# Performance work log

Measured on AMD Instinct MI355X. Metric: run time of the kernel, lower is better.

The kernel has to match this reference:

```python
import jax, jax.numpy as jnp
import numpy as np

N = 100000   # nodes
E = 1600000  # edges (avg degree 16)
F = 64       # input feature dim
H = 64       # hidden dim
O = 64       # conv output dim
C = 2        # channels (x.shape[1])
S = 1000     # number of subgraphs
M = 64       # nodes per subgraph
MH = 128     # MLP hidden
OUT = 1      # MLP output


def setup_inputs() -> dict:
    key = jax.random.key(0)
    ks = jax.random.split(key, 16)
    x = jax.random.normal(ks[0], (N, C, F), jnp.float32)
    edge_index = jax.random.randint(ks[1], (2, E), 0, N, dtype=jnp.int32)
    edge_weight = jax.random.uniform(ks[2], (E,), jnp.float32)
    subG_node = jax.random.randint(ks[3], (S, M), 0, N, dtype=jnp.int32)
    s1 = 1.0 / np.sqrt(F)
    s2 = 1.0 / np.sqrt(H)
    sm1 = 1.0 / np.sqrt(O)
    sm2 = 1.0 / np.sqrt(MH)
    return {
        "x": x,
        "edge_index": edge_index,
        "edge_weight": edge_weight,
        "subG_node": subG_node,
        "W1": jax.random.normal(ks[4], (F, H), jnp.float32) * s1,
        "b1": jnp.zeros((H,), jnp.float32),
        "gn_w": jnp.ones((H,), jnp.float32),
        "gn_b": jnp.zeros((H,), jnp.float32),
        "gn_ms": jnp.ones((H,), jnp.float32),
        "W2": jax.random.normal(ks[5], (H, O), jnp.float32) * s2,
        "b2": jnp.zeros((O,), jnp.float32),
        "mW1": jax.random.normal(ks[6], (O, MH), jnp.float32) * sm1,
        "mb1": jnp.zeros((MH,), jnp.float32),
        "mW2": jax.random.normal(ks[7], (MH, OUT), jnp.float32) * sm2,
        "mb2": jnp.zeros((OUT,), jnp.float32),
    }


def _graph_norm(h, w, b, ms, eps=1e-5):
    # PyG GraphNorm over all nodes (single graph): per-feature stats
    mean = jnp.mean(h, axis=0, keepdims=True)
    out = h - ms * mean
    var = jnp.mean(out * out, axis=0, keepdims=True)
    return w * out * jax.lax.rsqrt(var + eps) + b


def _gcn_layer(h, src, dst, norm, self_norm, W, b, n):
    # GCNConv: h' = D^-1/2 (A + I) D^-1/2 (h @ W) + b
    hw = h @ W                                   # [N, out]
    msg = norm[:, None] * hw[src]                # [E, out] gather
    agg = jax.ops.segment_sum(msg, dst, num_segments=n)  # scatter-add
    agg = agg + self_norm[:, None] * hw          # self-loop term
    return agg + b


def reference(x, edge_index, edge_weight, subG_node,
              W1, b1, gn_w, gn_b, gn_ms, W2, b2, mW1, mb1, mW2, mb2):
    n = x.shape[0]
    src, dst = edge_index[0], edge_index[1]
    # symmetric GCN normalization with self-loops of weight 1
    deg = jax.ops.segment_sum(edge_weight, dst, num_segments=n) + 1.0
    dinv = jax.lax.rsqrt(deg)
    norm = dinv[src] * edge_weight * dinv[dst]   # [E]
    self_norm = dinv * dinv                      # [N]

    def conv_channel(xc):  # xc: [N, F]
        h = _gcn_layer(xc, src, dst, norm, self_norm, W1, b1, n)
        h = _graph_norm(h, gn_w, gn_b, gn_ms)
        h = jax.nn.relu(h)
        return _gcn_layer(h, src, dst, norm, self_norm, W2, b2, n)

    emb = jax.vmap(conv_channel, in_axes=1, out_axes=1)(x)  # [N, C, O]
    emb = jnp.mean(emb, axis=1)                              # [N, O]
    # subgraph pooling: sp @ emb == sum of member-node embeddings
    pooled = jnp.sum(emb[subG_node], axis=1)                 # [S, O]
    h = jax.nn.relu(pooled @ mW1 + mb1)
    return h @ mW2 + mb2                                     # [S, 1]
```

## Files before the change

kernel.cpp:

```cpp
#include <hip/hip_runtime.h>
#include <hip/hip_fp16.h>


#define NNODES 100000
#define NEDGES 1600000
#define NSUB   1000
#define MSUB   64
#define MHID   128

#define WSHIFT 9
#define WIN    512
#define NWIN   ((NNODES + 511) >> 9)
#define NBLK   256
#define CHUNK  (NEDGES / NBLK)

typedef _Float16 f16x8 __attribute__((ext_vector_type(8)));
typedef float    f32x4 __attribute__((ext_vector_type(4)));


__global__ __launch_bounds__(256) void k_hist(const int* __restrict__ dst,
                                              int* __restrict__ block_counts,
                                              int* __restrict__ cursor,
                                              const int* __restrict__ subg,
                                              int* __restrict__ flags) {
    __shared__ int hist[NWIN];
    int t = threadIdx.x, b = blockIdx.x;
    if (b == 0 && t == 0) *cursor = 0;
    if (t < 250) flags[subg[b * 250 + t]] = 1;
    for (int i = t; i < NWIN; i += 256) hist[i] = 0;
    __syncthreads();
    int e0 = b * CHUNK;
    for (int e = e0 + t; e < e0 + CHUNK; e += 256)
        atomicAdd(&hist[dst[e] >> WSHIFT], 1);
    __syncthreads();
    for (int i = t; i < NWIN; i += 256) block_counts[b * NWIN + i] = hist[i];
}

__global__ __launch_bounds__(256) void k_off(const int* __restrict__ block_counts,
                                             int* __restrict__ cursor,
                                             int* __restrict__ win_base,
                                             int* __restrict__ win_lim,
                                             int* __restrict__ block_off,
                                             float* __restrict__ stats,
                                             unsigned* __restrict__ edges) {
    __shared__ int arr[256];
    __shared__ int red[256];
    __shared__ int base_s;
    int t = threadIdx.x, w = blockIdx.x;
    int own = block_counts[t * NWIN + w];
    arr[t] = own; red[t] = own;
    __syncthreads();
    for (int off = 128; off > 0; off >>= 1) {
        if (t < off) red[t] += red[t + off];
        __syncthreads();
    }
    if (t == 0) base_s = atomicAdd(cursor, red[0]);
    for (int off = 1; off < 256; off <<= 1) {
        int v = (t >= off) ? arr[t - off] : 0;
        __syncthreads();
        arr[t] += v;
        __syncthreads();
    }
    int base = base_s;
    block_off[t * NWIN + w] = base + arr[t] - own;
    if (t == 0) { win_base[w] = base; win_lim[w] = base + red[0]; }
    if (w == 0) {
        stats[t] = 0.0f; stats[t + 256] = 0.0f;
        if (t < 16) edges[NEDGES + t] = 0u;
    }
}

__global__ __launch_bounds__(256) void k_scatter(const int* __restrict__ src,
                                                 const int* __restrict__ dst,
                                                 const float* __restrict__ ew,
                                                 const int* __restrict__ block_off,
                                                 int2* __restrict__ esw) {
    __shared__ int myoff[NWIN];
    int t = threadIdx.x, b = blockIdx.x;
    for (int i = t; i < NWIN; i += 256) myoff[i] = block_off[b * NWIN + i];
    __syncthreads();
    int e0 = b * CHUNK;
    for (int e = e0 + t; e < e0 + CHUNK; e += 256) {
        int d = dst[e];
        int w = d >> WSHIFT;
        int pos = atomicAdd(&myoff[w], 1);
        int dl = d - (w << WSHIFT);
        esw[pos] = make_int2((dl << 17) | src[e], __float_as_int(ew[e]));
    }
}

__global__ __launch_bounds__(256) void k_fill2(const int* __restrict__ win_base,
                                               const int* __restrict__ win_lim,
                                               const int2* __restrict__ esw,
                                               unsigned* __restrict__ edges,
                                               int* __restrict__ row_ptr,
                                               int* __restrict__ cnt,
                                               float* __restrict__ dinv) {
    __shared__ int   cnt_l[WIN];
    __shared__ int   sc[WIN];
    __shared__ int   fill_l[WIN];
    __shared__ float degw[WIN];
    int t = threadIdx.x, w = blockIdx.x;
    #pragma unroll
    for (int i = t; i < WIN; i += 256) { cnt_l[i] = 0; fill_l[i] = 0; degw[i] = 0.f; }
    __syncthreads();
    int e0 = win_base[w], e1 = win_lim[w];
    for (int e = e0 + t; e < e1; e += 256) {
        int2 v = esw[e];
        int dl = ((unsigned)v.x) >> 17;
        atomicAdd(&cnt_l[dl], 1);
        atomicAdd(&degw[dl], __int_as_float(v.y));
    }
    __syncthreads();
    sc[t] = cnt_l[t]; sc[t + 256] = cnt_l[t + 256];
    __syncthreads();
    for (int off = 1; off < WIN; off <<= 1) {
        int v0 = (t >= off) ? sc[t - off] : 0;
        int v1 = (t + 256 >= off) ? sc[t + 256 - off] : 0;
        __syncthreads();
        sc[t] += v0; sc[t + 256] += v1;
        __syncthreads();
    }
    sc[t]       = e0 + sc[t]       - cnt_l[t];
    sc[t + 256] = e0 + sc[t + 256] - cnt_l[t + 256];
    __syncthreads();
    for (int e = e0 + t; e < e1; e += 256) {
        int2 v = esw[e];
        int dl = ((unsigned)v.x) >> 17;
        int pos = sc[dl] + atomicAdd(&fill_l[dl], 1);
        int wq = __float2int_rn(__int_as_float(v.y) * 32767.0f);
        edges[pos] = ((unsigned)wq << 17) | ((unsigned)v.x & 0x1FFFFu);
    }
    __syncthreads();
    #pragma unroll
    for (int i = t; i < WIN; i += 256) {
        int node = (w << WSHIFT) + i;
        if (node < NNODES) {
            row_ptr[node] = sc[i];
            cnt[node]     = cnt_l[i];
            dinv[node]    = rsqrtf(degw[i] + 1.0f);
        }
    }
}


template <bool TR>
__global__ __launch_bounds__(256) void k_gemm(const void* __restrict__ Xv,
                                              const float* __restrict__ Wg,
                                              const float* __restrict__ dinv,
                                              _Float16* __restrict__ Y,
                                              const float* __restrict__ stats,
                                              const float* __restrict__ gn_w,
                                              const float* __restrict__ gn_b,
                                              const float* __restrict__ gn_ms) {
    __shared__ __align__(16) _Float16 ob[4][16 * 72];
    int t = threadIdx.x;
    int wave = t >> 6, lane = t & 63;
    int m = lane & 15, q = lane >> 4;

    f16x8 bf[2][4];
    #pragma unroll
    for (int kb = 0; kb < 2; kb++)
        #pragma unroll
        for (int nt = 0; nt < 4; nt++)
            #pragma unroll
            for (int j = 0; j < 8; j++)
                bf[kb][nt][j] = (_Float16)Wg[(kb * 32 + q * 8 + j) * 64 + nt * 16 + m];

    float ca[16], cb[16];
    if constexpr (TR) {
        int c = m & 1;
        const float inv_n = 1.0f / (float)NNODES;
        #pragma unroll
        for (int kb = 0; kb < 2; kb++)
            #pragma unroll
            for (int j = 0; j < 8; j++) {
                int k = kb * 32 + q * 8 + j;
                int col = c * 64 + k;
                float mean = stats[col] * inv_n;
                float eh2  = stats[128 + col] * inv_n;
                float ms   = gn_ms[k];
                float mm   = ms * mean;
                float var  = eh2 - 2.0f * mm * mean + mm * mm;
                float A = gn_w[k] * rsqrtf(var + 1e-5f);
                ca[kb * 8 + j] = A;
                cb[kb * 8 + j] = gn_b[k] - A * mm;
            }
    }

    int tile = blockIdx.x * 4 + wave;
    int row0 = tile * 16;

    f16x8 af[2];
    if constexpr (!TR) {
        const float* xp = (const float*)Xv + (size_t)(row0 + m) * 64;
        #pragma unroll
        for (int kb = 0; kb < 2; kb++) {
            float4 u0 = *(const float4*)(xp + kb * 32 + q * 8);
            float4 u1 = *(const float4*)(xp + kb * 32 + q * 8 + 4);
            af[kb][0] = (_Float16)u0.x; af[kb][1] = (_Float16)u0.y;
            af[kb][2] = (_Float16)u0.z; af[kb][3] = (_Float16)u0.w;
            af[kb][4] = (_Float16)u1.x; af[kb][5] = (_Float16)u1.y;
            af[kb][6] = (_Float16)u1.z; af[kb][7] = (_Float16)u1.w;
        }
    } else {
        const _Float16* xp = (const _Float16*)Xv + (size_t)(row0 + m) * 64;
        #pragma unroll
        for (int kb = 0; kb < 2; kb++) {
            f16x8 v = *(const f16x8*)(xp + kb * 32 + q * 8);
            #pragma unroll
            for (int j = 0; j < 8; j++) {
                float f = (float)v[j];
                f = fmaxf(ca[kb * 8 + j] * f + cb[kb * 8 + j], 0.0f);
                af[kb][j] = (_Float16)f;
            }
        }
    }

    f32x4 acc[4];
    #pragma unroll
    for (int nt = 0; nt < 4; nt++) {
        acc[nt] = (f32x4){0.f, 0.f, 0.f, 0.f};
        acc[nt] = __builtin_amdgcn_mfma_f32_16x16x32_f16(af[0], bf[0][nt], acc[nt], 0, 0, 0);
        acc[nt] = __builtin_amdgcn_mfma_f32_16x16x32_f16(af[1], bf[1][nt], acc[nt], 0, 0, 0);
    }

    float dv[4];
    #pragma unroll
    for (int i = 0; i < 4; i++) dv[i] = dinv[(row0 + q * 4 + i) >> 1];

    _Float16* obw = ob[wave];
    #pragma unroll
    for (int nt = 0; nt < 4; nt++)
        #pragma unroll
        for (int i = 0; i < 4; i++)
            obw[(q * 4 + i) * 72 + nt * 16 + m] = (_Float16)(acc[nt][i] * dv[i]);
    __syncthreads();

    _Float16* yp = Y + (size_t)row0 * 64;
    #pragma unroll
    for (int s = 0; s < 2; s++) {
        int c8 = s * 64 + lane;
        int r = c8 >> 3, cg2 = c8 & 7;
        uint4 v = *(const uint4*)(obw + r * 72 + cg2 * 8);
        *(uint4*)(yp + (size_t)r * 64 + cg2 * 8) = v;
    }
}


template <bool USE_FLAGS>
__global__ __launch_bounds__(256) void k_prop(const __half* __restrict__ hw,
                                              const float* __restrict__ bias,
                                              const float* __restrict__ dinv,
                                              const int* __restrict__ row_ptr,
                                              const int* __restrict__ cnt,
                                              const unsigned* __restrict__ edges,
                                              const int* __restrict__ flags,
                                              __half* __restrict__ agg) {
    int t = threadIdx.x;
    int lane = t & 63;
    int n = __builtin_amdgcn_readfirstlane(blockIdx.x * 4 + (t >> 6));
    if (n >= NNODES) return;
    if constexpr (USE_FLAGS) { if (flags[n] != 1) return; }

    int f = lane * 2;
    int feat = f & 63;
    const float qs = 1.0f / 32767.0f;

    float2 bv = *(const float2*)(bias + feat);
    float dv = dinv[n];
    float2 self = __half22float2(*(const __half2*)(hw + (size_t)n * 128 + f));
    float acc0 = self.x;
    float acc1 = self.y;

    int start = row_ptr[n];
    int cn    = cnt[n];
    const unsigned* pp = edges + start;

    int full = cn & ~15;
    int p = 0;
    for (; p < full; p += 16) {
        unsigned e[16];
        #pragma unroll
        for (int i = 0; i < 16; i++) e[i] = pp[p + i];
        float2 h[16];
        #pragma unroll
        for (int i = 0; i < 16; i++) {
            int s = (int)(e[i] & 0x1FFFFu);
            h[i] = __half22float2(*(const __half2*)(hw + (size_t)s * 128 + f));
        }
        #pragma unroll
        for (int i = 0; i < 16; i++) {
            float w = (float)(e[i] >> 17) * qs;
            acc0 += w * h[i].x;
            acc1 += w * h[i].y;
        }
    }
    if (p < cn) {
        unsigned e[16];
        #pragma unroll
        for (int i = 0; i < 16; i++) e[i] = pp[p + i];
        float2 h[16];
        #pragma unroll
        for (int i = 0; i < 16; i++) {
            int s = (int)(e[i] & 0x1FFFFu);
            h[i] = __half22float2(*(const __half2*)(hw + (size_t)s * 128 + f));
        }
        #pragma unroll
        for (int i = 0; i < 16; i++) {
            float w = ((p + i) < cn) ? (float)(e[i] >> 17) * qs : 0.0f;
            acc0 += w * h[i].x;
            acc1 += w * h[i].y;
        }
    }

    *(__half2*)(agg + (size_t)n * 128 + f) =
        __floats2half2_rn(dv * acc0 + bv.x, dv * acc1 + bv.y);
}


__global__ __launch_bounds__(256) void k_stats(const __half* __restrict__ agg,
                                               float* __restrict__ stats) {
    __shared__ float ls[16][128];
    __shared__ float lq[16][128];
    int t = threadIdx.x;
    int cb = (t & 15) * 8;
    int rg = t >> 4;
    float s[8], q[8];
    #pragma unroll
    for (int i = 0; i < 8; i++) { s[i] = 0.f; q[i] = 0.f; }
    for (int r = blockIdx.x * 16 + rg; r < NNODES; r += gridDim.x * 16) {
        uint4 u = *(const uint4*)(agg + (size_t)r * 128 + cb);
        const __half2* h2 = (const __half2*)&u;
        #pragma unroll
        for (int i = 0; i < 4; i++) {
            float2 v = __half22float2(h2[i]);
            s[2*i]   += v.x; q[2*i]   += v.x * v.x;
            s[2*i+1] += v.y; q[2*i+1] += v.y * v.y;
        }
    }
    #pragma unroll
    for (int i = 0; i < 8; i++) { ls[rg][cb + i] = s[i]; lq[rg][cb + i] = q[i]; }
    __syncthreads();
    if (t < 128) {
        float a = 0.f, b = 0.f;
        #pragma unroll
        for (int g = 0; g < 16; g++) { a += ls[g][t]; b += lq[g][t]; }
        atomicAdd(&stats[t], a);
        atomicAdd(&stats[128 + t], b);
    }
}


__global__ __launch_bounds__(256) void k_head(const __half* __restrict__ agg,
                                              const int* __restrict__ subg,
                                              const float* __restrict__ mW1,
                                              const float* __restrict__ mb1,
                                              const float* __restrict__ mW2,
                                              const float* __restrict__ mb2,
                                              float* __restrict__ out) {
    __shared__ int   idx[64];
    __shared__ float pl[4][64];
    __shared__ float red[128];
    int s = blockIdx.x, t = threadIdx.x;
    if (t < 64) idx[t] = subg[s * 64 + t];
    __syncthreads();
    int j = t & 63, grp = t >> 6;
    float acc = 0.f;
    #pragma unroll
    for (int m = grp * 16; m < grp * 16 + 16; m++) {
        int n = idx[m];
        acc += __half2float(agg[(size_t)n * 128 + j]) +
               __half2float(agg[(size_t)n * 128 + 64 + j]);
    }
    pl[grp][j] = acc * 0.5f;
    __syncthreads();
    if (t < 64) pl[0][t] = pl[0][t] + pl[1][t] + pl[2][t] + pl[3][t];
    __syncthreads();
    if (t < 128) {
        float h = mb1[t];
        #pragma unroll
        for (int k = 0; k < 64; k++) h += pl[0][k] * mW1[k * 128 + t];
        h = fmaxf(h, 0.0f);
        red[t] = h * mW2[t];
    }
    __syncthreads();
    for (int off = 64; off > 0; off >>= 1) {
        if (t < off) red[t] += red[t + off];
        __syncthreads();
    }
    if (t == 0) out[s] = red[0] + mb2[0];
}


extern "C" void kernel_launch(void* const* d_in, const int* in_sizes, int n_in,
                              void* d_out, int out_size, void* d_ws, size_t ws_size,
                              hipStream_t stream) {
    const float* x     = (const float*)d_in[0];
    const int*   ei    = (const int*)d_in[1];
    const float* ew    = (const float*)d_in[2];
    const int*   subg  = (const int*)d_in[3];
    const float* W1    = (const float*)d_in[4];
    const float* b1    = (const float*)d_in[5];
    const float* gn_w  = (const float*)d_in[6];
    const float* gn_b  = (const float*)d_in[7];
    const float* gn_ms = (const float*)d_in[8];
    const float* W2    = (const float*)d_in[9];
    const float* b2    = (const float*)d_in[10];
    const float* mW1   = (const float*)d_in[11];
    const float* mb1   = (const float*)d_in[12];
    const float* mW2   = (const float*)d_in[13];
    const float* mb2   = (const float*)d_in[14];
    float* out = (float*)d_out;

    char* w = (char*)d_ws;
    size_t off = 0;
    auto alloc = [&](size_t bytes) {
        void* p = w + off;
        off = (off + bytes + 255) & ~(size_t)255;
        return p;
    };
    float*    dinv    = (float*)   alloc((size_t)NNODES * 4);
    int*      cnt     = (int*)     alloc((size_t)NNODES * 4);
    int*      row_ptr = (int*)     alloc((size_t)NNODES * 4);
    int*      flags   = (int*)     alloc((size_t)NNODES * 4);
    unsigned* edges   = (unsigned*)alloc(((size_t)NEDGES + 16) * 4);
    int2*     esw     = (int2*)    alloc((size_t)NEDGES * 8);
    __half*   hw      = (__half*)  alloc((size_t)NNODES * 128 * 2);
    __half*   agg     = (__half*)  alloc((size_t)NNODES * 128 * 2);
    float*    stats   = (float*)   alloc(512 * 4);
    int*      block_counts = (int*)alloc((size_t)NBLK * NWIN * 4);
    int*      block_off    = (int*)alloc((size_t)NBLK * NWIN * 4);
    int*      win_base     = (int*)alloc(NWIN * 4);
    int*      win_lim      = (int*)alloc(NWIN * 4);
    int*      cursor       = (int*)alloc(256);

    const int* src = ei;
    const int* dst = ei + NEDGES;

    k_hist   <<<NBLK, 256, 0, stream>>>(dst, block_counts, cursor, subg, flags);
    k_off    <<<NWIN, 256, 0, stream>>>(block_counts, cursor, win_base, win_lim,
                                        block_off, stats, edges);
    k_scatter<<<NBLK, 256, 0, stream>>>(src, dst, ew, block_off, esw);
    k_fill2  <<<NWIN, 256, 0, stream>>>(win_base, win_lim, esw, edges, row_ptr, cnt, dinv);

    k_gemm<false><<<3125, 256, 0, stream>>>(x, W1, dinv, (_Float16*)hw,
                                            nullptr, nullptr, nullptr, nullptr);
    k_prop<false><<<25000, 256, 0, stream>>>(hw, b1, dinv, row_ptr, cnt, edges,
                                             nullptr, agg);

    k_stats<<<512, 256, 0, stream>>>(agg, stats);

    k_gemm<true><<<3125, 256, 0, stream>>>(agg, W2, dinv, (_Float16*)hw,
                                           stats, gn_w, gn_b, gn_ms);
    k_prop<true><<<25000, 256, 0, stream>>>(hw, b2, dinv, row_ptr, cnt, edges,
                                            flags, agg);

    k_head<<<NSUB, 256, 0, stream>>>(agg, subg, mW1, mb1, mW2, mb2, out);
}
```

Baseline: 330.4 us.

## Merge edge binning into one kernel and fuse GraphNorm stats into propagation

Edge bucketing by destination window now runs in one kernel that claims space in fixed-capacity per-window slabs with global atomics. This replaces the separate histogram, offset-scan and scatter kernels. GraphNorm statistics are accumulated inside the first propagation kernel through shared-memory atomics into 64 partial slots, which removes the separate stats pass over agg. The second GEMM reduces those partials itself. The fixed WCAP capacity drops edges silently if a window overflows, and the early return for out-of-range nodes was removed while a __syncthreads now sits in the stats path.

Result: slower. 409.5 us (+23.9%).

```diff
diff --git a/kernel.cpp b/kernel.cpp
--- a/kernel.cpp
+++ b/kernel.cpp
@@ -5,12 +5,11 @@
 #define NNODES 100000
 #define NEDGES 1600000
 #define NSUB   1000
-#define MSUB   64
-#define MHID   128
 
 #define WSHIFT 9
 #define WIN    512
-#define NWIN   ((NNODES + 511) >> 9)
+#define NWIN   196
+#define WCAP   10240
 #define NBLK   256
 #define CHUNK  (NEDGES / NBLK)
 
@@ -18,79 +17,42 @@
 typedef float    f32x4 __attribute__((ext_vector_type(4)));
 
 
-__global__ __launch_bounds__(256) void k_hist(const int* __restrict__ dst,
-                                              int* __restrict__ block_counts,
-                                              int* __restrict__ cursor,
-                                              const int* __restrict__ subg,
-                                              int* __restrict__ flags) {
+__global__ __launch_bounds__(256) void k_bin(const int* __restrict__ src,
+                                             const int* __restrict__ dst,
+                                             const float* __restrict__ ew,
+                                             int* __restrict__ wcur,
+                                             int2* __restrict__ esw,
+                                             const int* __restrict__ subg,
+                                             int* __restrict__ flags) {
     __shared__ int hist[NWIN];
+    __shared__ int base[NWIN];
+    __shared__ int fill[NWIN];
     int t = threadIdx.x, b = blockIdx.x;
-    if (b == 0 && t == 0) *cursor = 0;
     if (t < 250) flags[subg[b * 250 + t]] = 1;
-    for (int i = t; i < NWIN; i += 256) hist[i] = 0;
+    for (int i = t; i < NWIN; i += 256) { hist[i] = 0; fill[i] = 0; }
     __syncthreads();
     int e0 = b * CHUNK;
     for (int e = e0 + t; e < e0 + CHUNK; e += 256)
         atomicAdd(&hist[dst[e] >> WSHIFT], 1);
     __syncthreads();
-    for (int i = t; i < NWIN; i += 256) block_counts[b * NWIN + i] = hist[i];
-}
-
-__global__ __launch_bounds__(256) void k_off(const int* __restrict__ block_counts,
-                                             int* __restrict__ cursor,
-                                             int* __restrict__ win_base,
-                                             int* __restrict__ win_lim,
-                                             int* __restrict__ block_off,
-                                             float* __restrict__ stats,
-                                             unsigned* __restrict__ edges) {
-    __shared__ int arr[256];
-    __shared__ int red[256];
-    __shared__ int base_s;
-    int t = threadIdx.x, w = blockIdx.x;
-    int own = block_counts[t * NWIN + w];
-    arr[t] = own; red[t] = own;
-    __syncthreads();
-    for (int off = 128; off > 0; off >>= 1) {
-        if (t < off) red[t] += red[t + off];
-        __syncthreads();
-    }
-    if (t == 0) base_s = atomicAdd(cursor, red[0]);
-    for (int off = 1; off < 256; off <<= 1) {
-        int v = (t >= off) ? arr[t - off] : 0;
-        __syncthreads();
-        arr[t] += v;
-        __syncthreads();
-    }
-    int base = base_s;
-    block_off[t * NWIN + w] = base + arr[t] - own;
-    if (t == 0) { win_base[w] = base; win_lim[w] = base + red[0]; }
-    if (w == 0) {
-        stats[t] = 0.0f; stats[t + 256] = 0.0f;
-        if (t < 16) edges[NEDGES + t] = 0u;
-    }
-}
-
-__global__ __launch_bounds__(256) void k_scatter(const int* __restrict__ src,
-                                                 const int* __restrict__ dst,
-                                                 const float* __restrict__ ew,
-                                                 const int* __restrict__ block_off,
-                                                 int2* __restrict__ esw) {
-    __shared__ int myoff[NWIN];
-    int t = threadIdx.x, b = blockIdx.x;
-    for (int i = t; i < NWIN; i += 256) myoff[i] = block_off[b * NWIN + i];
-    __syncthreads();
-    int e0 = b * CHUNK;
+    for (int i = t; i < NWIN; i += 256) {
+        int c = hist[i];
+        base[i] = c ? atomicAdd(&wcur[i], c) : 0;
+    }
+    __syncthreads();
     for (int e = e0 + t; e < e0 + CHUNK; e += 256) {
         int d = dst[e];
         int w = d >> WSHIFT;
-        int pos = atomicAdd(&myoff[w], 1);
-        int dl = d - (w << WSHIFT);
-        esw[pos] = make_int2((dl << 17) | src[e], __float_as_int(ew[e]));
-    }
-}
-
-__global__ __launch_bounds__(256) void k_fill2(const int* __restrict__ win_base,
-                                               const int* __restrict__ win_lim,
+        int pos = base[w] + atomicAdd(&fill[w], 1);
+        if (pos < WCAP) {
+            int dl = d - (w << WSHIFT);
+            esw[(size_t)w * WCAP + pos] =
+                make_int2((dl << 17) | src[e], __float_as_int(ew[e]));
+        }
+    }
+}
+
+__global__ __launch_bounds__(256) void k_fill2(const int* __restrict__ wcur,
                                                const int2* __restrict__ esw,
                                                unsigned* __restrict__ edges,
                                                int* __restrict__ row_ptr,
@@ -104,7 +66,9 @@
     #pragma unroll
     for (int i = t; i < WIN; i += 256) { cnt_l[i] = 0; fill_l[i] = 0; degw[i] = 0.f; }
     __syncthreads();
-    int e0 = win_base[w], e1 = win_lim[w];
+    int e0 = w * WCAP;
+    int count = wcur[w]; if (count > WCAP) count = WCAP;
+    int e1 = e0 + count;
     for (int e = e0 + t; e < e1; e += 256) {
         int2 v = esw[e];
         int dl = ((unsigned)v.x) >> 17;
@@ -149,14 +113,22 @@
                                               const float* __restrict__ Wg,
                                               const float* __restrict__ dinv,
                                               _Float16* __restrict__ Y,
-                                              const float* __restrict__ stats,
+                                              const float* __restrict__ partial,
                                               const float* __restrict__ gn_w,
                                               const float* __restrict__ gn_b,
                                               const float* __restrict__ gn_ms) {
     __shared__ __align__(16) _Float16 ob[4][16 * 72];
+    __shared__ float st[256];
     int t = threadIdx.x;
     int wave = t >> 6, lane = t & 63;
     int m = lane & 15, q = lane >> 4;
+
+    if constexpr (TR) {
+        float s = 0.f;
+        #pragma unroll 4
+        for (int j = 0; j < 64; j++) s += partial[j * 256 + t];
+        st[t] = s;
+    }
 
     f16x8 bf[2][4];
     #pragma unroll
@@ -169,6 +141,7 @@
 
     float ca[16], cb[16];
     if constexpr (TR) {
+        __syncthreads();
         int c = m & 1;
         const float inv_n = 1.0f / (float)NNODES;
         #pragma unroll
@@ -177,8 +150,8 @@
             for (int j = 0; j < 8; j++) {
                 int k = kb * 32 + q * 8 + j;
                 int col = c * 64 + k;
-                float mean = stats[col] * inv_n;
-                float eh2  = stats[128 + col] * inv_n;
+                float mean = st[col] * inv_n;
+                float eh2  = st[128 + col] * inv_n;
                 float ms   = gn_ms[k];
                 float mm   = ms * mean;
                 float var  = eh2 - 2.0f * mm * mean + mm * mm;
@@ -248,7 +221,7 @@
 }
 
 
-template <bool USE_FLAGS>
+template <bool USE_FLAGS, bool STATS>
 __global__ __launch_bounds__(256) void k_prop(const __half* __restrict__ hw,
                                               const float* __restrict__ bias,
                                               const float* __restrict__ dinv,
@@ -256,11 +229,18 @@
                                               const int* __restrict__ cnt,
                                               const unsigned* __restrict__ edges,
                                               const int* __restrict__ flags,
-                                              __half* __restrict__ agg) {
+                                              __half* __restrict__ agg,
+                                              float* __restrict__ partial) {
+    __shared__ float ssum[128];
+    __shared__ float ssq[128];
     int t = threadIdx.x;
     int lane = t & 63;
     int n = __builtin_amdgcn_readfirstlane(blockIdx.x * 4 + (t >> 6));
-    if (n >= NNODES) return;
+
+    if constexpr (STATS) {
+        if (t < 128) ssum[t] = 0.f; else ssq[t - 128] = 0.f;
+        __syncthreads();
+    }
     if constexpr (USE_FLAGS) { if (flags[n] != 1) return; }
 
     int f = lane * 2;
@@ -314,40 +294,16 @@
         }
     }
 
-    *(__half2*)(agg + (size_t)n * 128 + f) =
-        __floats2half2_rn(dv * acc0 + bv.x, dv * acc1 + bv.y);
-}
-
-
-__global__ __launch_bounds__(256) void k_stats(const __half* __restrict__ agg,
-                                               float* __restrict__ stats) {
-    __shared__ float ls[16][128];
-    __shared__ float lq[16][128];
-    int t = threadIdx.x;
-    int cb = (t & 15) * 8;
-    int rg = t >> 4;
-    float s[8], q[8];
-    #pragma unroll
-    for (int i = 0; i < 8; i++) { s[i] = 0.f; q[i] = 0.f; }
-    for (int r = blockIdx.x * 16 + rg; r < NNODES; r += gridDim.x * 16) {
-        uint4 u = *(const uint4*)(agg + (size_t)r * 128 + cb);
-        const __half2* h2 = (const __half2*)&u;
-        #pragma unroll
-        for (int i = 0; i < 4; i++) {
-            float2 v = __half22float2(h2[i]);
-            s[2*i]   += v.x; q[2*i]   += v.x * v.x;
-            s[2*i+1] += v.y; q[2*i+1] += v.y * v.y;
-        }
-    }
-    #pragma unroll
-    for (int i = 0; i < 8; i++) { ls[rg][cb + i] = s[i]; lq[rg][cb + i] = q[i]; }
-    __syncthreads();
-    if (t < 128) {
-        float a = 0.f, b = 0.f;
-        #pragma unroll
-        for (int g = 0; g < 16; g++) { a += ls[g][t]; b += lq[g][t]; }
-        atomicAdd(&stats[t], a);
-        atomicAdd(&stats[128 + t], b);
+    float r0 = dv * acc0 + bv.x;
+    float r1 = dv * acc1 + bv.y;
+    *(__half2*)(agg + (size_t)n * 128 + f) = __floats2half2_rn(r0, r1);
+
+    if constexpr (STATS) {
+        atomicAdd(&ssum[f], r0);     atomicAdd(&ssum[f + 1], r1);
+        atomicAdd(&ssq[f], r0 * r0); atomicAdd(&ssq[f + 1], r1 * r1);
+        __syncthreads();
+        float v = (t < 128) ? ssum[t] : ssq[t - 128];
+        atomicAdd(&partial[(blockIdx.x & 63) * 256 + t], v);
     }
 }
 
@@ -420,41 +376,35 @@
         off = (off + bytes + 255) & ~(size_t)255;
         return p;
     };
+    int*      wcur    = (int*)     alloc(NWIN * 4);
+    float*    partial = (float*)   alloc(64 * 256 * 4);
     float*    dinv    = (float*)   alloc((size_t)NNODES * 4);
     int*      cnt     = (int*)     alloc((size_t)NNODES * 4);
     int*      row_ptr = (int*)     alloc((size_t)NNODES * 4);
     int*      flags   = (int*)     alloc((size_t)NNODES * 4);
-    unsigned* edges   = (unsigned*)alloc(((size_t)NEDGES + 16) * 4);
-    int2*     esw     = (int2*)    alloc((size_t)NEDGES * 8);
+    unsigned* edges   = (unsigned*)alloc(((size_t)NWIN * WCAP + 64) * 4);
+    int2*     esw     = (int2*)    alloc((size_t)NWIN * WCAP * 8);
     __half*   hw      = (__half*)  alloc((size_t)NNODES * 128 * 2);
     __half*   agg     = (__half*)  alloc((size_t)NNODES * 128 * 2);
-    float*    stats   = (float*)   alloc(512 * 4);
-    int*      block_counts = (int*)alloc((size_t)NBLK * NWIN * 4);
-    int*      block_off    = (int*)alloc((size_t)NBLK * NWIN * 4);
-    int*      win_base     = (int*)alloc(NWIN * 4);
-    int*      win_lim      = (int*)alloc(NWIN * 4);
-    int*      cursor       = (int*)alloc(256);
 
     const int* src = ei;
     const int* dst = ei + NEDGES;
 
-    k_hist   <<<NBLK, 256, 0, stream>>>(dst, block_counts, cursor, subg, flags);
-    k_off    <<<NWIN, 256, 0, stream>>>(block_counts, cursor, win_base, win_lim,
-                                        block_off, stats, edges);
-    k_scatter<<<NBLK, 256, 0, stream>>>(src, dst, ew, block_off, esw);
-    k_fill2  <<<NWIN, 256, 0, stream>>>(win_base, win_lim, esw, edges, row_ptr, cnt, dinv);
+    size_t zspan = (size_t)((char*)(partial + 64 * 256) - (char*)wcur);
+    hipMemsetAsync(wcur, 0, zspan, stream);
+
+    k_bin  <<<NBLK, 256, 0, stream>>>(src, dst, ew, wcur, esw, subg, flags);
+    k_fill2<<<NWIN, 256, 0, stream>>>(wcur, esw, edges, row_ptr, cnt, dinv);
 
     k_gemm<false><<<3125, 256, 0, stream>>>(x, W1, dinv, (_Float16*)hw,
                                             nullptr, nullptr, nullptr, nullptr);
-    k_prop<false><<<25000, 256, 0, stream>>>(hw, b1, dinv, row_ptr, cnt, edges,
-                                             nullptr, agg);
-
-    k_stats<<<512, 256, 0, stream>>>(agg, stats);
+    k_prop<false, true><<<25000, 256, 0, stream>>>(hw, b1, dinv, row_ptr, cnt, edges,
+                                                   nullptr, agg, partial);
 
     k_gemm<true><<<3125, 256, 0, stream>>>(agg, W2, dinv, (_Float16*)hw,
-                                           stats, gn_w, gn_b, gn_ms);
-    k_prop<true><<<25000, 256, 0, stream>>>(hw, b2, dinv, row_ptr, cnt, edges,
-                                            flags, agg);
+                                           partial, gn_w, gn_b, gn_ms);
+    k_prop<true, false><<<25000, 256, 0, stream>>>(hw, b2, dinv, row_ptr, cnt, edges,
+                                                   flags, agg, nullptr);
 
     k_head<<<NSUB, 256, 0, stream>>>(agg, subg, mW1, mb1, mW2, mb2, out);
 }
```
